# Performance work log

Hardware: AMD Instinct MI355X
Metric: run time of the kernel (lower is better)

The kernel has to match this reference:

```python
import jax, jax.numpy as jnp
import numpy as np

DIM = 512
HEADS = 8
DIM_HEAD = 64
INNER = HEADS * DIM_HEAD  # 512


def setup_inputs() -> dict:
    key = jax.random.key(0)
    k1, k2, k3, k4 = jax.random.split(key, 4)
    x = jax.random.normal(k1, (2, 2048, DIM), dtype=jnp.float32)
    # nn.Linear weights are [out_features, in_features]
    w_qkv = jax.random.normal(k2, (INNER * 3, DIM), dtype=jnp.float32) * (1.0 / np.sqrt(DIM))
    w_out = jax.random.normal(k3, (DIM, INNER), dtype=jnp.float32) * (1.0 / np.sqrt(INNER))
    b_out = jax.random.normal(k4, (DIM,), dtype=jnp.float32) * 0.01
    return {"x": x, "w_qkv": w_qkv, "w_out": w_out, "b_out": b_out}


def reference(x, w_qkv, w_out, b_out):
    b, n, _ = x.shape
    qkv = x @ w_qkv.T  # (b, n, 3*inner)
    q, k, v = jnp.split(qkv, 3, axis=-1)
    # (b, n, inner) -> (b, h, n, dh)
    def to_heads(t):
        return t.reshape(b, n, HEADS, DIM_HEAD).transpose(0, 2, 1, 3)
    q, k, v = map(to_heads, (q, k, v))
    # Faithful to the torch code: softmax over head dim for q, over seq for k
    q = jax.nn.softmax(q, axis=-1)
    k = jax.nn.softmax(k, axis=-2)
    # torch einsum labels seq as i/j, head dim as d (contracted) -> [n, n] context
    context = jnp.einsum('bhid,bhjd->bhij', k, v)     # (b, h, n, n)
    out = jnp.einsum('bhij,bhie->bhje', context, q)   # (b, h, n, dh)
    out = out.transpose(0, 2, 1, 3).reshape(b, n, INNER)
    return out @ w_out.T + b_out
```

## Files before the change

### kernel.cpp

```cpp
#include <hip/hip_runtime.h>
#include <hip/hip_bf16.h>
#include <math.h>

#define BB   2
#define NN   2048
#define DIMM 512
#define HH   8
#define NC3  1536
#define BN   4096

typedef __attribute__((ext_vector_type(8))) short short8;
typedef __attribute__((ext_vector_type(4))) float f32x4;
typedef unsigned short u16t;

__device__ inline short bfc(float f) {
    __hip_bfloat16 h = __float2bfloat16(f);
    return *reinterpret_cast<short*>(&h);
}
__device__ inline float bf2f(u16t u) {
    return __uint_as_float(((unsigned)u) << 16);
}

#define SWZ(P) ((P) ^ ((((P) >> 7) & 3) << 4))

__global__ __launch_bounds__(256) void qkvgemm(
    const float* __restrict__ A, const float* __restrict__ Bw,
    u16t* __restrict__ QKV)
{
    __shared__ __align__(16) char smem[16384];

    const int tid  = threadIdx.x;
    const int wave = tid >> 6, lane = tid & 63;
    const int wr = wave >> 1, wc = wave & 1;

    int bid = blockIdx.y * gridDim.x + blockIdx.x;
    int swz = (bid & 7) * 48 + (bid >> 3);
    const int row0 = (swz & 31) * 128;
    const int c0   = (swz >> 5) * 128;

    float4 ra[2][2], rb[2][2];

#define QLOAD(KT) {                                                           \
    _Pragma("unroll")                                                         \
    for (int it = 0; it < 2; ++it) {                                          \
        int c = tid + it * 256, r = c >> 2, g = c & 3;                        \
        const float* pa = A + (size_t)(row0 + r) * DIMM + (KT) + g * 8;       \
        ra[it][0] = *(const float4*)pa; ra[it][1] = *(const float4*)(pa + 4); \
        const float* pb = Bw + (size_t)(c0 + r) * DIMM + (KT) + g * 8;        \
        rb[it][0] = *(const float4*)pb; rb[it][1] = *(const float4*)(pb + 4); \
    } }

#define QWRITE() {                                                            \
    _Pragma("unroll")                                                         \
    for (int it = 0; it < 2; ++it) {                                          \
        int P = (tid + it * 256) * 16;                                        \
        short8 av, bv;                                                        \
        av[0]=bfc(ra[it][0].x); av[1]=bfc(ra[it][0].y);                       \
        av[2]=bfc(ra[it][0].z); av[3]=bfc(ra[it][0].w);                       \
        av[4]=bfc(ra[it][1].x); av[5]=bfc(ra[it][1].y);                       \
        av[6]=bfc(ra[it][1].z); av[7]=bfc(ra[it][1].w);                       \
        bv[0]=bfc(rb[it][0].x); bv[1]=bfc(rb[it][0].y);                       \
        bv[2]=bfc(rb[it][0].z); bv[3]=bfc(rb[it][0].w);                       \
        bv[4]=bfc(rb[it][1].x); bv[5]=bfc(rb[it][1].y);                       \
        bv[6]=bfc(rb[it][1].z); bv[7]=bfc(rb[it][1].w);                       \
        *(short8*)(smem + SWZ(P)) = av;                                       \
        *(short8*)(smem + 8192 + SWZ(P)) = bv;                                \
    } }

    int rdA[4], rdB[4];
#pragma unroll
    for (int i = 0; i < 4; ++i) {
        int Pa = (wr * 64 + i * 16 + (lane & 15)) * 64 + (lane >> 4) * 16;
        rdA[i] = SWZ(Pa);
        int Pb = (wc * 64 + i * 16 + (lane & 15)) * 64 + (lane >> 4) * 16;
        rdB[i] = 8192 + SWZ(Pb);
    }

    f32x4 acc[4][4];
#pragma unroll
    for (int i = 0; i < 4; ++i)
#pragma unroll
        for (int j = 0; j < 4; ++j) acc[i][j] = (f32x4){0.f, 0.f, 0.f, 0.f};

    QLOAD(0);
    for (int kt = 0; kt < DIMM; kt += 32) {
        QWRITE();
        __syncthreads();
        if (kt + 32 < DIMM) QLOAD(kt + 32);

        short8 af[4], bfr[4];
#pragma unroll
        for (int i = 0; i < 4; ++i) {
            af[i]  = *(const short8*)(smem + rdA[i]);
            bfr[i] = *(const short8*)(smem + rdB[i]);
        }
#pragma unroll
        for (int i = 0; i < 4; ++i)
#pragma unroll
            for (int j = 0; j < 4; ++j)
                acc[i][j] = __builtin_amdgcn_mfma_f32_16x16x32_bf16(
                    af[i], bfr[j], acc[i][j], 0, 0, 0);
        __syncthreads();
    }
#undef QLOAD
#undef QWRITE

#pragma unroll
    for (int j = 0; j < 4; ++j) {
        int col = c0 + wc * 64 + j * 16 + (lane & 15);
#pragma unroll
        for (int i = 0; i < 4; ++i) {
#pragma unroll
            for (int r = 0; r < 4; ++r) {
                int row = row0 + wr * 64 + i * 16 + (lane >> 4) * 4 + r;
                QKV[(size_t)row * NC3 + col] = (u16t)bfc(acc[i][j][r]);
            }
        }
    }
}

#define TST 136

__global__ __launch_bounds__(512) void mpart(
    const u16t* __restrict__ QKV, float* __restrict__ Mp, float* __restrict__ ksump)
{
    __shared__ __align__(16) char sh[34816];
    u16t* ksT = (u16t*)sh;
    u16t* qsT = (u16t*)(sh + 17408);

    const int bh = blockIdx.x, ch = blockIdx.y;
    const int b = bh >> 3, h = bh & 7;
    const int tid = threadIdx.x;
    const u16t* base = QKV + ((size_t)b * NN + ch * 128) * NC3 + h * 64;

    const int k7 = tid & 7;
    const int d0 = k7 * 8;
    const int rr = tid >> 3;

#pragma unroll
    for (int pass = 0; pass < 2; ++pass) {
        int r = pass * 64 + rr;
        const u16t* rowp = base + (size_t)r * NC3 + d0;
        short8 qv = *(const short8*)(rowp);
        short8 kv = *(const short8*)(rowp + 512);
        float e[8]; float s = 0.f;
#pragma unroll
        for (int u = 0; u < 8; ++u) { e[u] = __expf(bf2f((u16t)qv[u])); s += e[u]; }
        s += __shfl_xor(s, 1); s += __shfl_xor(s, 2); s += __shfl_xor(s, 4);
        float inv = 1.0f / s;
        int gx = ((r >> 3) ^ k7) * 8 + (r & 7);
#pragma unroll
        for (int u = 0; u < 8; ++u)
            qsT[(d0 + u) * TST + gx] = (u16t)bfc(e[u] * inv);
#pragma unroll
        for (int u = 0; u < 8; ++u)
            ksT[(d0 + u) * TST + gx] = (u16t)bfc(__expf(bf2f((u16t)kv[u])));
    }
    __syncthreads();

    if (tid < 64) {
        float kss = 0.f;
#pragma unroll
        for (int gg = 0; gg < 16; ++gg) {
            short8 v = *(const short8*)(ksT + tid * TST + gg * 8);
#pragma unroll
            for (int u = 0; u < 8; ++u) kss += bf2f((u16t)v[u]);
        }
        ksump[(bh * 16 + ch) * 64 + tid] = kss;
    }

    const int wave = tid >> 6, lane = tid & 63;
    const int g = wave >> 1, kh = wave & 1;
    const int dl = lane & 15, kq = lane >> 4;
    const int d = g * 16 + dl;

    f32x4 acc[4];
#pragma unroll
    for (int j = 0; j < 4; ++j) acc[j] = (f32x4){0.f, 0.f, 0.f, 0.f};

#pragma unroll
    for (int ks2 = 0; ks2 < 2; ++ks2) {
        int kb = kh * 64 + ks2 * 32 + kq * 8;
        short8 af = *(const short8*)(ksT + d * TST + ((((kb >> 3) ^ (d >> 3))) << 3));
#pragma unroll
        for (int j = 0; j < 4; ++j) {
            int e = j * 16 + dl;
            short8 bfrj = *(const short8*)(qsT + e * TST + ((((kb >> 3) ^ (e >> 3))) << 3));
            acc[j] = __builtin_amdgcn_mfma_f32_16x16x32_bf16(af, bfrj, acc[j], 0, 0, 0);
        }
    }

    float* mp = Mp + ((size_t)((bh * 16 + ch) * 2 + kh)) * 4096;
#pragma unroll
    for (int j = 0; j < 4; ++j)
#pragma unroll
        for (int r = 0; r < 4; ++r)
            mp[(g * 16 + kq * 4 + r) * 64 + j * 16 + dl] = acc[j][r];
}

__global__ __launch_bounds__(256) void mreduce(
    const float* __restrict__ Mp, float* __restrict__ M)
{
    int bh = blockIdx.x;
    int idx = blockIdx.y * 256 + threadIdx.x;
    const float* p = Mp + (size_t)bh * 32 * 4096 + idx;
    float s = 0.f;
#pragma unroll
    for (int c = 0; c < 32; ++c) s += p[c * 4096];
    M[(size_t)bh * 4096 + idx] = s;
}

__global__ __launch_bounds__(256) void w2t(
    const float* __restrict__ M, const float* __restrict__ ksump,
    const float* __restrict__ w_out, u16t* __restrict__ W2T)
{
    __shared__ float kst[64];
    __shared__ float Ms[64][68];
    __shared__ float Wt[64][68];

    int bh = blockIdx.x, ot = blockIdx.y;
    int b = bh >> 3, h = bh & 7;
    int tid = threadIdx.x;
    int d = tid & 63, og = tid >> 6;

    if (tid < 64) {
        float s = 0.f;
#pragma unroll
        for (int c = 0; c < 16; ++c) s += ksump[(bh * 16 + c) * 64 + tid];
        kst[tid] = s;
    }
    for (int idx = tid; idx < 4096; idx += 256)
        Ms[idx >> 6][idx & 63] = M[(size_t)bh * 4096 + idx];
    {
        int o = tid >> 2, e0 = (tid & 3) * 16;
#pragma unroll
        for (int q = 0; q < 4; ++q)
            *(float4*)&Wt[o][e0 + q * 4] =
                *(const float4*)&w_out[(size_t)(ot * 64 + o) * DIMM + h * 64 + e0 + q * 4];
    }
    __syncthreads();

    float Mreg[64];
#pragma unroll
    for (int e4 = 0; e4 < 16; ++e4) {
        float4 v = *(const float4*)&Ms[d][e4 * 4];
        Mreg[e4 * 4 + 0] = v.x; Mreg[e4 * 4 + 1] = v.y;
        Mreg[e4 * 4 + 2] = v.z; Mreg[e4 * 4 + 3] = v.w;
    }
    float inv = 1.0f / kst[d];

#pragma unroll
    for (int oo = 0; oo < 16; ++oo) {
        int o = og * 16 + oo;
        float a = 0.f;
#pragma unroll
        for (int e4 = 0; e4 < 16; ++e4) {
            float4 wv = *(const float4*)&Wt[o][e4 * 4];
            a += wv.x * Mreg[e4 * 4 + 0] + wv.y * Mreg[e4 * 4 + 1]
               + wv.z * Mreg[e4 * 4 + 2] + wv.w * Mreg[e4 * 4 + 3];
        }
        W2T[((size_t)b * DIMM + ot * 64 + o) * DIMM + h * 64 + d] = (u16t)bfc(a * inv);
    }
}

__device__ inline void gll16(const u16t* gp, void* lp) {
    __builtin_amdgcn_global_load_lds(
        (const __attribute__((address_space(1))) void*)gp,
        (__attribute__((address_space(3))) void*)lp,
        16, 0, 0);
}

__global__ __launch_bounds__(256) void outgemm(
    const u16t* __restrict__ Aq, const u16t* __restrict__ W2T,
    const float* __restrict__ bias, float* __restrict__ Out)
{
    __shared__ __align__(16) char smem[24576];

    const int tid  = threadIdx.x;
    const int wave = tid >> 6, lane = tid & 63;
    const int wr = wave >> 1, wc = wave & 1;

    int bid = blockIdx.y * gridDim.x + blockIdx.x;
    int swz = (bid & 7) * 32 + (bid >> 3);
    const int row0 = (swz & 31) * 128;
    const int c0   = (swz >> 5) * 64;
    const u16t* Bp = W2T + (size_t)(row0 >> 11) * (DIMM * DIMM);

    size_t gA[2], gB;
#pragma unroll
    for (int j = 0; j < 2; ++j) {
        int c = wave * 2 + j;
        int gi = SWZ((c * 64 + lane) * 16) >> 4;
        int row = gi >> 2, col = (gi & 3) * 8;
        gA[j] = (size_t)(row0 + row) * NC3 + col;
    }
    {
        int gi = SWZ((wave * 64 + lane) * 16) >> 4;
        int row = gi >> 2, col = (gi & 3) * 8;
        gB = (size_t)(c0 + row) * DIMM + col;
    }

    int rdA[4], rdB[2];
#pragma unroll
    for (int i = 0; i < 4; ++i) {
        int Pa = (wr * 64 + i * 16 + (lane & 15)) * 64 + (lane >> 4) * 16;
        rdA[i] = SWZ(Pa);
    }
#pragma unroll
    for (int j = 0; j < 2; ++j) {
        int Pb = (wc * 32 + j * 16 + (lane & 15)) * 64 + (lane >> 4) * 16;
        rdB[j] = 8192 + SWZ(Pb);
    }

#define OSTAGE(BUF, KT) {                                                     \
    char* sb = smem + (BUF) * 12288;                                          \
    _Pragma("unroll")                                                         \
    for (int j = 0; j < 2; ++j)                                               \
        gll16(Aq + gA[j] + (KT), sb + (wave * 2 + j) * 1024);                 \
    gll16(Bp + gB + (KT), sb + 8192 + wave * 1024);                           \
    }

    f32x4 acc[4][2];
#pragma unroll
    for (int i = 0; i < 4; ++i)
#pragma unroll
        for (int j = 0; j < 2; ++j) acc[i][j] = (f32x4){0.f, 0.f, 0.f, 0.f};

    OSTAGE(0, 0);
    for (int t = 0; t < 16; ++t) {
        __syncthreads();
        if (t < 15) OSTAGE((t + 1) & 1, (t + 1) * 32);
        const char* rb = smem + (t & 1) * 12288;
        short8 af[4], bfr[2];
#pragma unroll
        for (int i = 0; i < 4; ++i) af[i]  = *(const short8*)(rb + rdA[i]);
#pragma unroll
        for (int j = 0; j < 2; ++j) bfr[j] = *(const short8*)(rb + rdB[j]);
#pragma unroll
        for (int i = 0; i < 4; ++i)
#pragma unroll
            for (int j = 0; j < 2; ++j)
                acc[i][j] = __builtin_amdgcn_mfma_f32_16x16x32_bf16(
                    af[i], bfr[j], acc[i][j], 0, 0, 0);
    }
#undef OSTAGE

#pragma unroll
    for (int j = 0; j < 2; ++j) {
        int col = c0 + wc * 32 + j * 16 + (lane & 15);
        float bb = bias[col];
#pragma unroll
        for (int i = 0; i < 4; ++i) {
#pragma unroll
            for (int r = 0; r < 4; ++r) {
                int row = row0 + wr * 64 + i * 16 + (lane >> 4) * 4 + r;
                Out[(size_t)row * DIMM + col] = acc[i][j][r] + bb;
            }
        }
    }
}

extern "C" void kernel_launch(void* const* d_in, const int* in_sizes, int n_in,
                              void* d_out, int out_size, void* d_ws, size_t ws_size,
                              hipStream_t stream)
{
    const float* x     = (const float*)d_in[0];
    const float* w_qkv = (const float*)d_in[1];
    const float* w_out = (const float*)d_in[2];
    const float* b_out = (const float*)d_in[3];
    float* out = (float*)d_out;

    char* w = (char*)d_ws;
    u16t*  QKV  = (u16t*) (w);
    float* Mp   = (float*)(w + 12582912);
    float* ksum = (float*)(w + 20971520);
    float* Mm   = (float*)(w + 21037056);
    u16t*  W2T  = (u16t*) (w + 21299200);

    qkvgemm<<<dim3(32, 12), 256, 0, stream>>>(x, w_qkv, QKV);

    mpart<<<dim3(16, 16), 512, 0, stream>>>(QKV, Mp, ksum);

    mreduce<<<dim3(16, 16), 256, 0, stream>>>(Mp, Mm);

    w2t<<<dim3(16, 8), 256, 0, stream>>>(Mm, ksum, w_out, W2T);

    outgemm<<<dim3(32, 8), 256, 0, stream>>>(QKV + 1024, W2T, b_out, out);
}
```

Baseline: 49.14 us.

## Pre-convert QKV GEMM inputs to bf16, double-buffer via direct LDS loads, fuse mreduce

A new kernel converts x and w_qkv to bf16 once. The QKV GEMM can then stream tiles straight into double-buffered LDS with global_load_lds, which removes the per-tile register conversion and one barrier per iteration. The separate mreduce kernel is also removed, and its 32-way partial sum is folded into w2t's shared-memory load. The cost is an extra launch, more workspace traffic for the bf16 copies, and each w2t block (8 per head) now repeats the same reduction.

```diff
diff --git a/kernel.cpp b/kernel.cpp
--- a/kernel.cpp
+++ b/kernel.cpp
@@ -23,11 +23,33 @@
 
 #define SWZ(P) ((P) ^ ((((P) >> 7) & 3) << 4))
 
+__device__ inline void gll16(const u16t* gp, void* lp) {
+    __builtin_amdgcn_global_load_lds(
+        (const __attribute__((address_space(1))) void*)gp,
+        (__attribute__((address_space(3))) void*)lp,
+        16, 0, 0);
+}
+
+__global__ __launch_bounds__(256) void cvt_bf16(
+    const float* __restrict__ x, const float* __restrict__ wq,
+    u16t* __restrict__ xb, u16t* __restrict__ wqb)
+{
+    int t = blockIdx.x * 256 + threadIdx.x;
+    const float4* src; ushort4* dst; int i;
+    if (t < 524288) { src = (const float4*)x;  dst = (ushort4*)xb;  i = t; }
+    else            { src = (const float4*)wq; dst = (ushort4*)wqb; i = t - 524288; }
+    float4 v = src[i];
+    ushort4 u;
+    u.x = (u16t)bfc(v.x); u.y = (u16t)bfc(v.y);
+    u.z = (u16t)bfc(v.z); u.w = (u16t)bfc(v.w);
+    dst[i] = u;
+}
+
 __global__ __launch_bounds__(256) void qkvgemm(
-    const float* __restrict__ A, const float* __restrict__ Bw,
+    const u16t* __restrict__ A, const u16t* __restrict__ Bw,
     u16t* __restrict__ QKV)
 {
-    __shared__ __align__(16) char smem[16384];
+    __shared__ __align__(16) char smem[32768];
 
     const int tid  = threadIdx.x;
     const int wave = tid >> 6, lane = tid & 63;
@@ -38,34 +60,16 @@
     const int row0 = (swz & 31) * 128;
     const int c0   = (swz >> 5) * 128;
 
-    float4 ra[2][2], rb[2][2];
-
-#define QLOAD(KT) {                                                           \
-    _Pragma("unroll")                                                         \
-    for (int it = 0; it < 2; ++it) {                                          \
-        int c = tid + it * 256, r = c >> 2, g = c & 3;                        \
-        const float* pa = A + (size_t)(row0 + r) * DIMM + (KT) + g * 8;       \
-        ra[it][0] = *(const float4*)pa; ra[it][1] = *(const float4*)(pa + 4); \
-        const float* pb = Bw + (size_t)(c0 + r) * DIMM + (KT) + g * 8;        \
-        rb[it][0] = *(const float4*)pb; rb[it][1] = *(const float4*)(pb + 4); \
-    } }
-
-#define QWRITE() {                                                            \
-    _Pragma("unroll")                                                         \
-    for (int it = 0; it < 2; ++it) {                                          \
-        int P = (tid + it * 256) * 16;                                        \
-        short8 av, bv;                                                        \
-        av[0]=bfc(ra[it][0].x); av[1]=bfc(ra[it][0].y);                       \
-        av[2]=bfc(ra[it][0].z); av[3]=bfc(ra[it][0].w);                       \
-        av[4]=bfc(ra[it][1].x); av[5]=bfc(ra[it][1].y);                       \
-        av[6]=bfc(ra[it][1].z); av[7]=bfc(ra[it][1].w);                       \
-        bv[0]=bfc(rb[it][0].x); bv[1]=bfc(rb[it][0].y);                       \
-        bv[2]=bfc(rb[it][0].z); bv[3]=bfc(rb[it][0].w);                       \
-        bv[4]=bfc(rb[it][1].x); bv[5]=bfc(rb[it][1].y);                       \
-        bv[6]=bfc(rb[it][1].z); bv[7]=bfc(rb[it][1].w);                       \
-        *(short8*)(smem + SWZ(P)) = av;                                       \
-        *(short8*)(smem + 8192 + SWZ(P)) = bv;                                \
-    } }
+    size_t gA[2], gB[2];
+#pragma unroll
+    for (int j = 0; j < 2; ++j) {
+        int c = wave * 2 + j;
+        int X = (c * 64 + lane) * 16;
+        int gi = SWZ(X) >> 4;
+        int row = gi >> 2, col = (gi & 3) * 8;
+        gA[j] = (size_t)(row0 + row) * DIMM + col;
+        gB[j] = (size_t)(c0   + row) * DIMM + col;
+    }
 
     int rdA[4], rdB[4];
 #pragma unroll
@@ -76,23 +80,30 @@
         rdB[i] = 8192 + SWZ(Pb);
     }
 
+#define QSTAGE(BUF, KT) {                                                     \
+    char* sb = smem + (BUF) * 16384;                                          \
+    _Pragma("unroll")                                                         \
+    for (int j = 0; j < 2; ++j) {                                             \
+        gll16(A  + gA[j] + (KT), sb + (wave * 2 + j) * 1024);                 \
+        gll16(Bw + gB[j] + (KT), sb + 8192 + (wave * 2 + j) * 1024);          \
+    } }
+
     f32x4 acc[4][4];
 #pragma unroll
     for (int i = 0; i < 4; ++i)
 #pragma unroll
         for (int j = 0; j < 4; ++j) acc[i][j] = (f32x4){0.f, 0.f, 0.f, 0.f};
 
-    QLOAD(0);
-    for (int kt = 0; kt < DIMM; kt += 32) {
-        QWRITE();
+    QSTAGE(0, 0);
+    for (int t = 0; t < 16; ++t) {
         __syncthreads();
-        if (kt + 32 < DIMM) QLOAD(kt + 32);
-
+        if (t < 15) QSTAGE((t + 1) & 1, (t + 1) * 32);
+        const char* rb = smem + (t & 1) * 16384;
         short8 af[4], bfr[4];
 #pragma unroll
         for (int i = 0; i < 4; ++i) {
-            af[i]  = *(const short8*)(smem + rdA[i]);
-            bfr[i] = *(const short8*)(smem + rdB[i]);
+            af[i]  = *(const short8*)(rb + rdA[i]);
+            bfr[i] = *(const short8*)(rb + rdB[i]);
         }
 #pragma unroll
         for (int i = 0; i < 4; ++i)
@@ -100,10 +111,8 @@
             for (int j = 0; j < 4; ++j)
                 acc[i][j] = __builtin_amdgcn_mfma_f32_16x16x32_bf16(
                     af[i], bfr[j], acc[i][j], 0, 0, 0);
-        __syncthreads();
-    }
-#undef QLOAD
-#undef QWRITE
+    }
+#undef QSTAGE
 
 #pragma unroll
     for (int j = 0; j < 4; ++j) {
@@ -198,20 +207,8 @@
             mp[(g * 16 + kq * 4 + r) * 64 + j * 16 + dl] = acc[j][r];
 }
 
-__global__ __launch_bounds__(256) void mreduce(
-    const float* __restrict__ Mp, float* __restrict__ M)
-{
-    int bh = blockIdx.x;
-    int idx = blockIdx.y * 256 + threadIdx.x;
-    const float* p = Mp + (size_t)bh * 32 * 4096 + idx;
-    float s = 0.f;
-#pragma unroll
-    for (int c = 0; c < 32; ++c) s += p[c * 4096];
-    M[(size_t)bh * 4096 + idx] = s;
-}
-
 __global__ __launch_bounds__(256) void w2t(
-    const float* __restrict__ M, const float* __restrict__ ksump,
+    const float* __restrict__ Mp, const float* __restrict__ ksump,
     const float* __restrict__ w_out, u16t* __restrict__ W2T)
 {
     __shared__ float kst[64];
@@ -229,8 +226,13 @@
         for (int c = 0; c < 16; ++c) s += ksump[(bh * 16 + c) * 64 + tid];
         kst[tid] = s;
     }
-    for (int idx = tid; idx < 4096; idx += 256)
-        Ms[idx >> 6][idx & 63] = M[(size_t)bh * 4096 + idx];
+    for (int idx = tid; idx < 4096; idx += 256) {
+        const float* p = Mp + (size_t)bh * 32 * 4096 + idx;
+        float s = 0.f;
+#pragma unroll
+        for (int c = 0; c < 32; ++c) s += p[c * 4096];
+        Ms[idx >> 6][idx & 63] = s;
+    }
     {
         int o = tid >> 2, e0 = (tid & 3) * 16;
 #pragma unroll
@@ -261,13 +263,6 @@
         }
         W2T[((size_t)b * DIMM + ot * 64 + o) * DIMM + h * 64 + d] = (u16t)bfc(a * inv);
     }
-}
-
-__device__ inline void gll16(const u16t* gp, void* lp) {
-    __builtin_amdgcn_global_load_lds(
-        (const __attribute__((address_space(1))) void*)gp,
-        (__attribute__((address_space(3))) void*)lp,
-        16, 0, 0);
 }
 
 __global__ __launch_bounds__(256) void outgemm(
@@ -371,19 +366,20 @@
     float* out = (float*)d_out;
 
     char* w = (char*)d_ws;
-    u16t*  QKV  = (u16t*) (w);
-    float* Mp   = (float*)(w + 12582912);
-    float* ksum = (float*)(w + 20971520);
-    float* Mm   = (float*)(w + 21037056);
-    u16t*  W2T  = (u16t*) (w + 21299200);
-
-    qkvgemm<<<dim3(32, 12), 256, 0, stream>>>(x, w_qkv, QKV);
+    u16t*  xb   = (u16t*) (w);
+    u16t*  wqb  = (u16t*) (w + 4194304);
+    u16t*  QKV  = (u16t*) (w + 5767168);
+    float* Mp   = (float*)(w + 18350080);
+    float* ksum = (float*)(w + 26738688);
+    u16t*  W2T  = (u16t*) (w + 26804224);
+
+    cvt_bf16<<<dim3(2816), 256, 0, stream>>>(x, w_qkv, xb, wqb);
+
+    qkvgemm<<<dim3(32, 12), 256, 0, stream>>>(xb, wqb, QKV);
 
     mpart<<<dim3(16, 16), 512, 0, stream>>>(QKV, Mp, ksum);
 
-    mreduce<<<dim3(16, 16), 256, 0, stream>>>(Mp, Mm);
-
-    w2t<<<dim3(16, 8), 256, 0, stream>>>(Mm, ksum, w_out, W2T);
+    w2t<<<dim3(16, 8), 256, 0, stream>>>(Mp, ksum, w_out, W2T);
 
     outgemm<<<dim3(32, 8), 256, 0, stream>>>(QKV + 1024, W2T, b_out, out);
 }
```

New measurement: 57.33 us. +16.7%, slower.
